# Optimization experiments

Measured on AMD Instinct MI355X. Metric: run time of the kernel, lower is better.

Reference implementation:

```python
import jax, jax.numpy as jnp
import numpy as np

LABELS_NUM_COUNT = [500000, 120000, 80000, 45000, 30000, 250000, 15000, 9000,
                    60000, 7000, 180000, 22000, 11000, 95000, 5000, 40000]
B, W = 2097152, 16  # batch, num_classes


def _build_penalty_matrix():
    c = np.asarray(LABELS_NUM_COUNT, dtype=np.float32)
    P = np.maximum(c[:, None], c[None, :]) / (c[:, None] + c[None, :])
    np.fill_diagonal(P, 1.0)
    return jnp.asarray(P)  # [W, W]


def setup_inputs() -> dict:
    key = jax.random.key(0)
    k1, k2 = jax.random.split(key)
    predict = jax.random.normal(k1, (B, W), dtype=jnp.float32)
    target = jax.random.normal(k2, (B, W), dtype=jnp.float32)
    return {"predict": predict, "target": target,
            "penalty_matrix": _build_penalty_matrix()}


def reference(predict, target, penalty_matrix):
    # `logpredict` in the original is actually softmax(predict).
    probs = jax.nn.softmax(predict, axis=-1)              # [B, W]
    pre = jnp.argmax(predict, axis=-1)                    # [B] predicted class
    tar = jnp.argmax(target, axis=-1)                     # [B] target class
    # scatter_ writes 1 at the predicted slot, then the loop overwrites it with
    # penalty[tar, pre] on mismatch or 0 on match -> net weight is:
    w = jnp.where(pre == tar, jnp.float32(0.0), penalty_matrix[tar, pre])  # [B]
    # sum(onehot * probs, -1) == probs at the predicted class
    p_at_pre = jnp.take_along_axis(probs, pre[:, None], axis=-1)[:, 0]     # [B]
    return jnp.mean(w * p_at_pre)
```

## Files before the change

### kernel.cpp

```cpp
#include <hip/hip_runtime.h>

#define NROWS 2097152
#define W 16
#define TPB 256
#define BLOCKS 4096
#define NTHREADS (BLOCKS * TPB)
#define RPT (NROWS / NTHREADS)

typedef float f32x4 __attribute__((ext_vector_type(4)));

__device__ __forceinline__ int argmax16(const float* v, float& mout)
{
    float a0 = fmaxf(v[0],  v[1]),  a1 = fmaxf(v[2],  v[3]);
    float a2 = fmaxf(v[4],  v[5]),  a3 = fmaxf(v[6],  v[7]);
    float a4 = fmaxf(v[8],  v[9]),  a5 = fmaxf(v[10], v[11]);
    float a6 = fmaxf(v[12], v[13]), a7 = fmaxf(v[14], v[15]);
    float b0 = fmaxf(a0, a1), b1 = fmaxf(a2, a3);
    float b2 = fmaxf(a4, a5), b3 = fmaxf(a6, a7);
    float m  = fmaxf(fmaxf(b0, b1), fmaxf(b2, b3));
    unsigned mask = 0u;
#pragma unroll
    for (int j = 0; j < 16; ++j) mask |= (v[j] == m) ? (1u << j) : 0u;
    mout = m;
    return __ffs(mask) - 1;
}

__global__ __launch_bounds__(TPB) void cel_weight_kernel(
    const float* __restrict__ predict,
    const float* __restrict__ target,
    const float* __restrict__ penalty,
    float* __restrict__ out)
{
    __shared__ float s_pen[W * W];
    __shared__ float s_part[TPB / 64];

    const int tid = threadIdx.x;
    s_pen[tid] = penalty[tid];
    __syncthreads();

    const int gid = blockIdx.x * TPB + tid;

    f32x4 pb[RPT][4], tb[RPT][4];
#pragma unroll
    for (int k = 0; k < RPT; ++k) {
        const f32x4* prow = (const f32x4*)predict + (size_t)(gid + k * NTHREADS) * 4;
        const f32x4* trow = (const f32x4*)target  + (size_t)(gid + k * NTHREADS) * 4;
#pragma unroll
        for (int j = 0; j < 4; ++j) pb[k][j] = __builtin_nontemporal_load(&prow[j]);
#pragma unroll
        for (int j = 0; j < 4; ++j) tb[k][j] = __builtin_nontemporal_load(&trow[j]);
    }
    __builtin_amdgcn_sched_barrier(0);

    float acc = 0.0f;

#pragma unroll
    for (int k = 0; k < RPT; ++k) {
        float pv[W], tv[W];
#pragma unroll
        for (int j = 0; j < 4; ++j) {
#pragma unroll
            for (int e = 0; e < 4; ++e) {
                pv[j * 4 + e] = pb[k][j][e];
                tv[j * 4 + e] = tb[k][j][e];
            }
        }

        float pmax, tmax;
        const int pidx = argmax16(pv, pmax);
        const int tidx = argmax16(tv, tmax);

        float s = 0.0f;
#pragma unroll
        for (int j = 0; j < W; ++j) s += __expf(pv[j] - pmax);

        const float w = s_pen[tidx * W + pidx];
        acc += (pidx == tidx) ? 0.0f : w / s;
    }

#pragma unroll
    for (int off = 32; off > 0; off >>= 1)
        acc += __shfl_down(acc, off);

    const int lane = tid & 63;
    const int wid  = tid >> 6;
    if (lane == 0) s_part[wid] = acc;
    __syncthreads();

    if (tid == 0) {
        float tot = s_part[0] + s_part[1] + s_part[2] + s_part[3];
        atomicAdd(out, tot * (1.0f / (float)NROWS));
    }
}

extern "C" void kernel_launch(void* const* d_in, const int* in_sizes, int n_in,
                              void* d_out, int out_size, void* d_ws, size_t ws_size,
                              hipStream_t stream)
{
    const float* predict = (const float*)d_in[0];
    const float* target  = (const float*)d_in[1];
    const float* penalty = (const float*)d_in[2];
    float* out = (float*)d_out;

    hipMemsetAsync(out, 0, sizeof(float) * out_size, stream);

    dim3 grid(BLOCKS), block(TPB);
    cel_weight_kernel<<<grid, block, 0, stream>>>(predict, target, penalty, out);
}
```

Baseline: 290.0 us.

## Double-buffer row loads across four rows per thread with half the blocks

Halves the grid so each thread handles four rows instead of two, and replaces the load-everything-then-compute structure with a two-slot ping-pong buffer: the next row's loads are issued before the current row is computed. Launch bounds now request four blocks per CU. The aim is to overlap memory latency with the softmax and argmax math while using fewer registers than holding every row at once. The risk is fewer loads in flight per thread at the start, plus fewer total waves, which could reduce memory-level parallelism on a bandwidth-bound kernel.

Result: faster. 278.7 us (-3.9%).

```diff
diff --git a/kernel.cpp b/kernel.cpp
--- a/kernel.cpp
+++ b/kernel.cpp
@@ -3,7 +3,7 @@
 #define NROWS 2097152
 #define W 16
 #define TPB 256
-#define BLOCKS 4096
+#define BLOCKS 2048
 #define NTHREADS (BLOCKS * TPB)
 #define RPT (NROWS / NTHREADS)
 
@@ -25,7 +25,35 @@
     return __ffs(mask) - 1;
 }
 
-__global__ __launch_bounds__(TPB) void cel_weight_kernel(
+__device__ __forceinline__ void load_row(const f32x4* __restrict__ base, int r,
+                                         f32x4 v[4])
+{
+    const f32x4* p = base + (size_t)r * 4;
+#pragma unroll
+    for (int j = 0; j < 4; ++j) v[j] = __builtin_nontemporal_load(&p[j]);
+}
+
+__device__ __forceinline__ float row_term(const f32x4 p[4], const f32x4 t[4],
+                                          const float* __restrict__ s_pen)
+{
+    float pv[W], tv[W];
+#pragma unroll
+    for (int j = 0; j < 4; ++j)
+#pragma unroll
+        for (int e = 0; e < 4; ++e) {
+            pv[4 * j + e] = p[j][e];
+            tv[4 * j + e] = t[j][e];
+        }
+    float pmax, tmax;
+    const int pidx = argmax16(pv, pmax);
+    const int tidx = argmax16(tv, tmax);
+    float s = 0.0f;
+#pragma unroll
+    for (int j = 0; j < W; ++j) s += __expf(pv[j] - pmax);
+    return (pidx == tidx) ? 0.0f : s_pen[tidx * W + pidx] / s;
+}
+
+__global__ __launch_bounds__(TPB, 4) void cel_weight_kernel(
     const float* __restrict__ predict,
     const float* __restrict__ target,
     const float* __restrict__ penalty,
@@ -39,44 +67,28 @@
     __syncthreads();
 
     const int gid = blockIdx.x * TPB + tid;
+    const f32x4* __restrict__ P4 = (const f32x4*)predict;
+    const f32x4* __restrict__ T4 = (const f32x4*)target;
 
-    f32x4 pb[RPT][4], tb[RPT][4];
-#pragma unroll
-    for (int k = 0; k < RPT; ++k) {
-        const f32x4* prow = (const f32x4*)predict + (size_t)(gid + k * NTHREADS) * 4;
-        const f32x4* trow = (const f32x4*)target  + (size_t)(gid + k * NTHREADS) * 4;
-#pragma unroll
-        for (int j = 0; j < 4; ++j) pb[k][j] = __builtin_nontemporal_load(&prow[j]);
-#pragma unroll
-        for (int j = 0; j < 4; ++j) tb[k][j] = __builtin_nontemporal_load(&trow[j]);
-    }
-    __builtin_amdgcn_sched_barrier(0);
+    f32x4 pA[4], tA[4], pB[4], tB[4];
+
+    load_row(P4, gid + 0 * NTHREADS, pA);
+    load_row(T4, gid + 0 * NTHREADS, tA);
+    load_row(P4, gid + 1 * NTHREADS, pB);
+    load_row(T4, gid + 1 * NTHREADS, tB);
 
     float acc = 0.0f;
+    acc += row_term(pA, tA, s_pen);
 
-#pragma unroll
-    for (int k = 0; k < RPT; ++k) {
-        float pv[W], tv[W];
-#pragma unroll
-        for (int j = 0; j < 4; ++j) {
-#pragma unroll
-            for (int e = 0; e < 4; ++e) {
-                pv[j * 4 + e] = pb[k][j][e];
-                tv[j * 4 + e] = tb[k][j][e];
-            }
-        }
+    load_row(P4, gid + 2 * NTHREADS, pA);
+    load_row(T4, gid + 2 * NTHREADS, tA);
+    acc += row_term(pB, tB, s_pen);
 
-        float pmax, tmax;
-        const int pidx = argmax16(pv, pmax);
-        const int tidx = argmax16(tv, tmax);
+    load_row(P4, gid + 3 * NTHREADS, pB);
+    load_row(T4, gid + 3 * NTHREADS, tB);
+    acc += row_term(pA, tA, s_pen);
 
-        float s = 0.0f;
-#pragma unroll
-        for (int j = 0; j < W; ++j) s += __expf(pv[j] - pmax);
-
-        const float w = s_pen[tidx * W + pidx];
-        acc += (pidx == tidx) ? 0.0f : w / s;
-    }
+    acc += row_term(pB, tB, s_pen);
 
 #pragma unroll
     for (int off = 32; off > 0; off >>= 1)
```
